# Performance work log

Measured on AMD Instinct MI355X. Metric: run time of the kernel, lower is better.

## Reference

```python
import jax, jax.numpy as jnp
import numpy as np

B, S, D, H, C = 64, 512, 768, 768, 5


def setup_inputs() -> dict:
    key = jax.random.key(0)
    ks = jax.random.split(key, 7)
    return {
        "hidden_states": jax.random.normal(ks[0], (B, S, D), jnp.float32),
        "mask": jnp.ones((B, S), dtype=bool),
        # Dense(hidden_size, relu)
        "W1": jax.random.normal(ks[1], (D, H), jnp.float32) * 0.02,
        "b1": jnp.zeros((H,), jnp.float32),
        # CRF inner dense -> potentials over num_classes
        "W2": jax.random.normal(ks[2], (H, C), jnp.float32) * 0.02,
        "b2": jnp.zeros((C,), jnp.float32),
        # CRF transition matrix and boundary energies (tfa use_boundary=True)
        "chain_kernel": jax.random.normal(ks[3], (C, C), jnp.float32) * 0.1,
        "left_boundary": jax.random.normal(ks[4], (C,), jnp.float32) * 0.1,
        "right_boundary": jax.random.normal(ks[5], (C,), jnp.float32) * 0.1,
    }


def viterbi_decode(potentials, trans):
    """potentials: [B,S,C], trans: [C,C] -> decoded tags [B,S] int32."""
    pot_t = jnp.swapaxes(potentials, 0, 1)  # [S,B,C]

    def fwd_step(alpha, pot):
        scores = alpha[:, :, None] + trans[None]      # [B,C_prev,C_cur]
        bp = jnp.argmax(scores, axis=1)               # [B,C]
        alpha = jnp.max(scores, axis=1) + pot         # [B,C]
        return alpha, bp

    alpha, bps = jax.lax.scan(fwd_step, pot_t[0], pot_t[1:])  # bps: [S-1,B,C]
    last = jnp.argmax(alpha, axis=-1).astype(jnp.int32)       # [B]

    def back_step(tag, bp):
        prev = jnp.take_along_axis(bp, tag[:, None], axis=1)[:, 0].astype(jnp.int32)
        return prev, prev

    _, tags = jax.lax.scan(back_step, last, bps, reverse=True)  # [S-1,B]
    decoded = jnp.concatenate([jnp.swapaxes(tags, 0, 1), last[:, None]], axis=1)
    return decoded


def reference(hidden_states, mask, W1, b1, W2, b2, chain_kernel,
              left_boundary, right_boundary):
    # Dense + ReLU (dropout is identity at inference / training=False)
    h = jax.nn.relu(jnp.einsum('bsd,dh->bsh', hidden_states, W1) + b1)
    # CRF inner dense -> unary potentials
    pot = jnp.einsum('bsh,hc->bsc', h, W2) + b2
    # boundary energies at first / last timestep (mask is full-length here)
    pot = pot.at[:, 0].add(left_boundary).at[:, -1].add(right_boundary)
    seq_length = jnp.sum(mask.astype(jnp.int32), axis=1)
    decoded = viterbi_decode(pot, chain_kernel)
    return decoded, pot, seq_length, chain_kernel
```

## Files before the change

### kernel.cpp

```cpp
#include <hip/hip_runtime.h>

#define B_  64
#define S_  512
#define D_  768
#define H_  768
#define C_  5
#define M_  (B_ * S_)

typedef float f32x4 __attribute__((ext_vector_type(4)));
typedef short short8 __attribute__((ext_vector_type(8)));

#define W1T_ELEMS (D_ * H_)
#define XBF_ELEMS (M_ * D_)

#define PX_BLOCKS   (XBF_ELEMS / (256 * 8))
#define PW_BLOCKS   ((D_ / 32) * (H_ / 32))
#define PI_BLOCKS   ((M_ * C_ + 255) / 256)

__device__ __forceinline__ unsigned short f2bf(float f) {
    unsigned int u = __float_as_uint(f);
    u += 0x7FFFu + ((u >> 16) & 1u);
    return (unsigned short)(u >> 16);
}

__global__ __launch_bounds__(256) void prep_all_kernel(
    const float* __restrict__ X, const float* __restrict__ W1,
    const float* __restrict__ b2, const float* __restrict__ lb,
    const float* __restrict__ rb,
    unsigned short* __restrict__ xbf, unsigned short* __restrict__ w1t,
    float* __restrict__ pot)
{
    __shared__ float t[32][33];
    const int bid = blockIdx.x;
    const int tid = threadIdx.x;

    if (bid < PX_BLOCKS) {
        const size_t i0 = ((size_t)bid * 256 + tid) * 8;
        const float4 a = *(const float4*)(X + i0);
        const float4 b = *(const float4*)(X + i0 + 4);
        union { unsigned short u[8]; uint4 v; } o;
        o.u[0] = f2bf(a.x); o.u[1] = f2bf(a.y); o.u[2] = f2bf(a.z); o.u[3] = f2bf(a.w);
        o.u[4] = f2bf(b.x); o.u[5] = f2bf(b.y); o.u[6] = f2bf(b.z); o.u[7] = f2bf(b.w);
        *(uint4*)(xbf + i0) = o.v;
    } else if (bid < PX_BLOCKS + PW_BLOCKS) {
        const int b2i = bid - PX_BLOCKS;
        const int bx = b2i % (H_ / 32);
        const int by = b2i / (H_ / 32);
        const int lx = tid & 31, ly = tid >> 5;
        #pragma unroll
        for (int j = 0; j < 4; ++j)
            t[ly + 8 * j][lx] = W1[(by * 32 + ly + 8 * j) * H_ + bx * 32 + lx];
        __syncthreads();
        #pragma unroll
        for (int j = 0; j < 4; ++j)
            w1t[(size_t)(bx * 32 + ly + 8 * j) * D_ + by * 32 + lx] = f2bf(t[lx][ly + 8 * j]);
    } else {
        const int idx = (bid - PX_BLOCKS - PW_BLOCKS) * 256 + tid;
        if (idx < M_ * C_) {
            const int c = idx % C_;
            const int tt = (idx / C_) & (S_ - 1);
            float v = b2[c];
            if (tt == 0)      v += lb[c];
            if (tt == S_ - 1) v += rb[c];
            pot[idx] = v;
        }
    }
}

__global__ __launch_bounds__(256) void prep_w1_kernel(
    const float* __restrict__ W1, unsigned short* __restrict__ w1t)
{
    __shared__ float t[32][33];
    const int bx = blockIdx.x, by = blockIdx.y;
    const int lx = threadIdx.x & 31, ly = threadIdx.x >> 5;
    #pragma unroll
    for (int j = 0; j < 4; ++j)
        t[ly + 8 * j][lx] = W1[(by * 32 + ly + 8 * j) * H_ + bx * 32 + lx];
    __syncthreads();
    #pragma unroll
    for (int j = 0; j < 4; ++j)
        w1t[(size_t)(bx * 32 + ly + 8 * j) * D_ + by * 32 + lx] = f2bf(t[lx][ly + 8 * j]);
}

__global__ __launch_bounds__(256) void init_pot_kernel(
    const float* __restrict__ b2, const float* __restrict__ lb,
    const float* __restrict__ rb, float* __restrict__ pot)
{
    const int idx = blockIdx.x * 256 + threadIdx.x;
    if (idx < M_ * C_) {
        const int c = idx % C_;
        const int t = (idx / C_) & (S_ - 1);
        float v = b2[c];
        if (t == 0)      v += lb[c];
        if (t == S_ - 1) v += rb[c];
        pot[idx] = v;
    }
}

__device__ __forceinline__ void gload16(const void* g, void* l) {
    __builtin_amdgcn_global_load_lds(
        (const __attribute__((address_space(1))) unsigned int*)g,
        (__attribute__((address_space(3))) unsigned int*)l, 16, 0, 0);
}

__global__ __launch_bounds__(256, 4) void gemm_sb_kernel(
    const unsigned short* __restrict__ xbf,
    const unsigned short* __restrict__ w1t,
    const float* __restrict__ b1,
    const float* __restrict__ W2,
    float* __restrict__ pot)
{
    __shared__ __align__(16) unsigned short Asm[8192];
    __shared__ __align__(16) unsigned short Bsm[8192];

    const int tid  = threadIdx.x;
    const int lane = tid & 63, w = tid >> 6;
    const int wm   = w >> 1, wn = w & 1;
    const int i15  = lane & 15, quad = lane >> 4;

    const int bid = blockIdx.x;
    const int r8 = bid & 7, q8 = bid >> 3;
    const int nb = q8 % 6, mhi = q8 / 6;
    const int m0 = (mhi * 8 + r8) * 128;
    const int n0 = nb * 128;

    const unsigned short* gA[2];
    const unsigned short* gB[2];
    int lofs[2];
    #pragma unroll
    for (int i = 0; i < 2; ++i) {
        const int g = 2 * w + i;
        gA[i] = xbf + (size_t)(m0 + g * 16 + i15) * D_ + quad * 8;
        gB[i] = w1t + (size_t)(n0 + g * 16 + i15) * D_ + quad * 8;
        lofs[i] = g * 512;
    }

    f32x4 acc[4][4];
    #pragma unroll
    for (int mi = 0; mi < 4; ++mi)
        #pragma unroll
        for (int ni = 0; ni < 4; ++ni)
            acc[mi][ni] = (f32x4){0.f, 0.f, 0.f, 0.f};

    #define KITERS (D_ / 64)
    for (int kt = 0; kt < KITERS; ++kt) {
        __syncthreads();
        #pragma unroll
        for (int i = 0; i < 2; ++i) {
            gload16(gA[i],      &Asm[lofs[i]]);
            gload16(gA[i] + 32, &Asm[4096 + lofs[i]]);
            gload16(gB[i],      &Bsm[lofs[i]]);
            gload16(gB[i] + 32, &Bsm[4096 + lofs[i]]);
            gA[i] += 64; gB[i] += 64;
        }
        __syncthreads();

        #pragma unroll
        for (int c = 0; c < 2; ++c) {
            const int cb = c * 4096;
            short8 af[4], bfr[4];
            #pragma unroll
            for (int mi = 0; mi < 4; ++mi)
                af[mi] = *(const short8*)&Asm[cb + (wm * 4 + mi) * 512 + quad * 128 + i15 * 8];
            #pragma unroll
            for (int ni = 0; ni < 4; ++ni)
                bfr[ni] = *(const short8*)&Bsm[cb + (wn * 4 + ni) * 512 + quad * 128 + i15 * 8];
            #pragma unroll
            for (int ni = 0; ni < 4; ++ni)
                #pragma unroll
                for (int mi = 0; mi < 4; ++mi)
                    acc[mi][ni] = __builtin_amdgcn_mfma_f32_16x16x32_bf16(
                        af[mi], bfr[ni], acc[mi][ni], 0, 0, 0);
        }
    }
    __syncthreads();

    float* pp = (float*)&Asm[0];

    float b1v[4], w2v[4][C_];
    #pragma unroll
    for (int ni = 0; ni < 4; ++ni) {
        const int col = n0 + wn * 64 + ni * 16 + i15;
        b1v[ni] = b1[col];
        #pragma unroll
        for (int cc = 0; cc < C_; ++cc) w2v[ni][cc] = W2[col * C_ + cc];
    }

    #pragma unroll
    for (int mi = 0; mi < 4; ++mi) {
        float ps[4][C_];
        #pragma unroll
        for (int r = 0; r < 4; ++r)
            #pragma unroll
            for (int cc = 0; cc < C_; ++cc) ps[r][cc] = 0.f;

        #pragma unroll
        for (int ni = 0; ni < 4; ++ni)
            #pragma unroll
            for (int r = 0; r < 4; ++r) {
                float h = acc[mi][ni][r] + b1v[ni];
                h = h > 0.f ? h : 0.f;
                #pragma unroll
                for (int cc = 0; cc < C_; ++cc)
                    ps[r][cc] = fmaf(h, w2v[ni][cc], ps[r][cc]);
            }

        #pragma unroll
        for (int off = 1; off < 16; off <<= 1)
            #pragma unroll
            for (int r = 0; r < 4; ++r)
                #pragma unroll
                for (int cc = 0; cc < C_; ++cc)
                    ps[r][cc] += __shfl_xor(ps[r][cc], off, 64);

        if (i15 == 0) {
            #pragma unroll
            for (int r = 0; r < 4; ++r) {
                const int row = wm * 64 + mi * 16 + quad * 4 + r;
                #pragma unroll
                for (int cc = 0; cc < C_; ++cc)
                    pp[(wn * 128 + row) * C_ + cc] = ps[r][cc];
            }
        }
    }
    __syncthreads();

    for (int idx = tid; idx < 128 * C_; idx += 256) {
        const int row = idx / C_, cc = idx % C_;
        atomicAdd(&pot[(size_t)(m0 + row) * C_ + cc],
                  pp[row * C_ + cc] + pp[(128 + row) * C_ + cc]);
    }
}

__global__ __launch_bounds__(256) void gemm_bf16_kernel(
    const float* __restrict__ X,
    const unsigned short* __restrict__ w1t,
    const float* __restrict__ b1,
    const float* __restrict__ W2,
    float* __restrict__ pot)
{
    __shared__ __align__(16) float          Asm[128 * 32];
    __shared__ __align__(16) unsigned short Bsm[128 * 32];
    __shared__ float pp[2][128][C_];

    const int tid  = threadIdx.x;
    const int lane = tid & 63, w = tid >> 6;
    const int wm   = w >> 1, wn = w & 1;
    const int i15  = lane & 15, quad = lane >> 4;

    const int bid = blockIdx.x;
    const int r8 = bid & 7, q8 = bid >> 3;
    const int nb = q8 % 6, mhi = q8 / 6;
    const int m0 = (mhi * 8 + r8) * 128;
    const int n0 = nb * 128;

    const float* gA[4];
    float* lA[4];
    const unsigned short* gB[2];
    unsigned short* lB[2];
    #pragma unroll
    for (int i = 0; i < 4; ++i) {
        const int a = 4 * w + i, g = a >> 1, h = a & 1;
        gA[i] = X + (size_t)(m0 + g * 16 + i15) * D_ + (4 * h + quad) * 4;
        lA[i] = &Asm[g * 512 + h * 256];
    }
    #pragma unroll
    for (int i = 0; i < 2; ++i) {
        const int b = 2 * w + i;
        gB[i] = w1t + (size_t)(n0 + b * 16 + i15) * D_ + quad * 8;
        lB[i] = &Bsm[b * 512];
    }

    f32x4 acc[4][4];
    #pragma unroll
    for (int mi = 0; mi < 4; ++mi)
        #pragma unroll
        for (int ni = 0; ni < 4; ++ni)
            acc[mi][ni] = (f32x4){0.f, 0.f, 0.f, 0.f};

    for (int kt = 0; kt < D_ / 32; ++kt) {
        __syncthreads();
        #pragma unroll
        for (int i = 0; i < 4; ++i) { gload16(gA[i], lA[i]); gA[i] += 32; }
        #pragma unroll
        for (int i = 0; i < 2; ++i) { gload16(gB[i], lB[i]); gB[i] += 32; }
        __syncthreads();

        short8 af[4];
        #pragma unroll
        for (int mi = 0; mi < 4; ++mi) {
            const int row = wm * 64 + mi * 16 + i15;
            const int base = (row >> 4) * 512 + (row & 15) * 4 + quad * 128;
            const f32x4 lo = *(const f32x4*)&Asm[base];
            const f32x4 hi = *(const f32x4*)&Asm[base + 64];
            float f[8];
            *(f32x4*)&f[0] = lo; *(f32x4*)&f[4] = hi;
            union { short8 s; unsigned short u[8]; } cv;
            #pragma unroll
            for (int j = 0; j < 8; ++j) cv.u[j] = f2bf(f[j]);
            af[mi] = cv.s;
        }
        short8 bfr[4];
        #pragma unroll
        for (int ni = 0; ni < 4; ++ni) {
            const int row = wn * 64 + ni * 16 + i15;
            bfr[ni] = *(const short8*)&Bsm[(row >> 4) * 512 + quad * 128 + (row & 15) * 8];
        }
        #pragma unroll
        for (int ni = 0; ni < 4; ++ni)
            #pragma unroll
            for (int mi = 0; mi < 4; ++mi)
                acc[mi][ni] = __builtin_amdgcn_mfma_f32_16x16x32_bf16(
                    af[mi], bfr[ni], acc[mi][ni], 0, 0, 0);
    }

    float b1v[4], w2v[4][C_];
    #pragma unroll
    for (int ni = 0; ni < 4; ++ni) {
        const int col = n0 + wn * 64 + ni * 16 + i15;
        b1v[ni] = b1[col];
        #pragma unroll
        for (int cc = 0; cc < C_; ++cc) w2v[ni][cc] = W2[col * C_ + cc];
    }

    #pragma unroll
    for (int mi = 0; mi < 4; ++mi) {
        float ps[4][C_];
        #pragma unroll
        for (int r = 0; r < 4; ++r)
            #pragma unroll
            for (int cc = 0; cc < C_; ++cc) ps[r][cc] = 0.f;

        #pragma unroll
        for (int ni = 0; ni < 4; ++ni)
            #pragma unroll
            for (int r = 0; r < 4; ++r) {
                float h = acc[mi][ni][r] + b1v[ni];
                h = h > 0.f ? h : 0.f;
                #pragma unroll
                for (int cc = 0; cc < C_; ++cc)
                    ps[r][cc] = fmaf(h, w2v[ni][cc], ps[r][cc]);
            }

        #pragma unroll
        for (int off = 1; off < 16; off <<= 1)
            #pragma unroll
            for (int r = 0; r < 4; ++r)
                #pragma unroll
                for (int cc = 0; cc < C_; ++cc)
                    ps[r][cc] += __shfl_xor(ps[r][cc], off, 64);

        if (i15 == 0) {
            #pragma unroll
            for (int r = 0; r < 4; ++r) {
                const int row = wm * 64 + mi * 16 + quad * 4 + r;
                #pragma unroll
                for (int cc = 0; cc < C_; ++cc)
                    pp[wn][row][cc] = ps[r][cc];
            }
        }
    }
    __syncthreads();

    for (int idx = tid; idx < 128 * C_; idx += 256) {
        const int row = idx / C_, cc = idx % C_;
        atomicAdd(&pot[(size_t)(m0 + row) * C_ + cc],
                  pp[0][row][cc] + pp[1][row][cc]);
    }
}

#define FBK 8
#define FLDS 132
__global__ __launch_bounds__(256) void gemm_relu_pot_kernel(
    const float* __restrict__ X, const float* __restrict__ W1,
    const float* __restrict__ b1, const float* __restrict__ W2,
    float* __restrict__ pot)
{
    __shared__ float As[FBK * FLDS];
    __shared__ float Bs[FBK * FLDS];
    __shared__ float w2s[128][C_];

    const int tid = threadIdx.x;
    const int tx = tid & 15, ty = tid >> 4;
    const int m0 = blockIdx.y * 128, n0 = blockIdx.x * 128;

    for (int idx = tid; idx < 128 * C_; idx += 256)
        w2s[idx / C_][idx % C_] = W2[(n0 + idx / C_) * C_ + idx % C_];

    float acc[2][2][4][4];
    #pragma unroll
    for (int a = 0; a < 2; ++a)
        #pragma unroll
        for (int b = 0; b < 2; ++b)
            #pragma unroll
            for (int i = 0; i < 4; ++i)
                #pragma unroll
                for (int j = 0; j < 4; ++j) acc[a][b][i][j] = 0.f;

    const int arow = tid >> 1, aq = tid & 1;
    const int brow = tid >> 5, bq = tid & 31;
    const float* Aptr = X + (m0 + arow) * D_ + aq * 4;
    const float* Bptr = W1 + brow * H_ + n0 + bq * 4;

    for (int kt = 0; kt < D_; kt += FBK) {
        const float4 avv = *(const float4*)Aptr;
        const float4 bvv = *(const float4*)Bptr;
        __syncthreads();
        As[(aq * 4 + 0) * FLDS + arow] = avv.x;
        As[(aq * 4 + 1) * FLDS + arow] = avv.y;
        As[(aq * 4 + 2) * FLDS + arow] = avv.z;
        As[(aq * 4 + 3) * FLDS + arow] = avv.w;
        *(float4*)&Bs[brow * FLDS + bq * 4] = bvv;
        __syncthreads();
        #pragma unroll
        for (int k = 0; k < FBK; ++k) {
            const float4 a0 = *(const float4*)&As[k * FLDS + (ty << 2)];
            const float4 a1 = *(const float4*)&As[k * FLDS + 64 + (ty << 2)];
            const float4 b0 = *(const float4*)&Bs[k * FLDS + (tx << 2)];
            const float4 b1r = *(const float4*)&Bs[k * FLDS + 64 + (tx << 2)];
            const float ar[2][4] = {{a0.x,a0.y,a0.z,a0.w},{a1.x,a1.y,a1.z,a1.w}};
            const float br[2][4] = {{b0.x,b0.y,b0.z,b0.w},{b1r.x,b1r.y,b1r.z,b1r.w}};
            #pragma unroll
            for (int ri = 0; ri < 2; ++ri)
                #pragma unroll
                for (int i = 0; i < 4; ++i)
                    #pragma unroll
                    for (int rj = 0; rj < 2; ++rj)
                        #pragma unroll
                        for (int j = 0; j < 4; ++j)
                            acc[ri][rj][i][j] = fmaf(ar[ri][i], br[rj][j], acc[ri][rj][i][j]);
        }
        Aptr += FBK;
        Bptr += FBK * H_;
    }

    float ps[2][4][C_];
    #pragma unroll
    for (int ri = 0; ri < 2; ++ri)
        #pragma unroll
        for (int i = 0; i < 4; ++i)
            #pragma unroll
            for (int cc = 0; cc < C_; ++cc) ps[ri][i][cc] = 0.f;

    #pragma unroll
    for (int rj = 0; rj < 2; ++rj)
        #pragma unroll
        for (int j = 0; j < 4; ++j) {
            const int nl = rj * 64 + (tx << 2) + j;
            const float bj = b1[n0 + nl];
            float w2c[C_];
            #pragma unroll
            for (int cc = 0; cc < C_; ++cc) w2c[cc] = w2s[nl][cc];
            #pragma unroll
            for (int ri = 0; ri < 2; ++ri)
                #pragma unroll
                for (int i = 0; i < 4; ++i) {
                    float h = acc[ri][rj][i][j] + bj;
                    h = h > 0.f ? h : 0.f;
                    #pragma unroll
                    for (int cc = 0; cc < C_; ++cc)
                        ps[ri][i][cc] = fmaf(h, w2c[cc], ps[ri][i][cc]);
                }
        }

    #pragma unroll
    for (int off = 1; off < 16; off <<= 1)
        #pragma unroll
        for (int ri = 0; ri < 2; ++ri)
            #pragma unroll
            for (int i = 0; i < 4; ++i)
                #pragma unroll
                for (int cc = 0; cc < C_; ++cc)
                    ps[ri][i][cc] += __shfl_xor(ps[ri][i][cc], off, 64);

    if (tx == 0)
        #pragma unroll
        for (int ri = 0; ri < 2; ++ri)
            #pragma unroll
            for (int i = 0; i < 4; ++i) {
                const int m = m0 + ri * 64 + (ty << 2) + i;
                #pragma unroll
                for (int cc = 0; cc < C_; ++cc)
                    atomicAdd(&pot[m * C_ + cc], ps[ri][i][cc]);
            }
}

__global__ __launch_bounds__(64) void viterbi_kernel(
    const float* __restrict__ pot, const float* __restrict__ trans,
    const int* __restrict__ mask, float* __restrict__ decoded,
    float* __restrict__ seqlen, float* __restrict__ chain_out)
{
    const int b = blockIdx.x;
    const int lane = threadIdx.x;

    __shared__ float pl[S_ * C_];
    __shared__ unsigned int bpk[S_];
    __shared__ unsigned int gseg[64];
    __shared__ int bt[64];
    __shared__ int dec_s[S_];
    __shared__ int s_last;

    const float* pb = pot + b * (S_ * C_);
    for (int i = lane; i < S_ * C_; i += 64) pl[i] = pb[i];

    int mcnt = 0;
    const int* mb = mask + b * S_;
    for (int i = lane; i < S_; i += 64) mcnt += (mb[i] != 0) ? 1 : 0;
    #pragma unroll
    for (int off = 32; off >= 1; off >>= 1) mcnt += __shfl_xor(mcnt, off, 64);

    if (b == 0 && lane < C_ * C_) chain_out[lane] = trans[lane];

    float tr[C_][C_];
    #pragma unroll
    for (int p = 0; p < C_; ++p)
        #pragma unroll
        for (int c = 0; c < C_; ++c) tr[p][c] = trans[p * C_ + c];

    __syncthreads();

    const float NEG = -1.0e30f;

    float G[C_][C_];
    #pragma unroll
    for (int c = 0; c < C_; ++c)
        #pragma unroll
        for (int p = 0; p < C_; ++p) G[c][p] = (c == p) ? 0.f : NEG;

    for (int j = 1; j <= 8; ++j) {
        const int t = 8 * lane + j;
        if (t < S_) {
            float ng[C_][C_];
            #pragma unroll
            for (int c = 0; c < C_; ++c) {
                const float pc = pl[t * C_ + c];
                #pragma unroll
                for (int p = 0; p < C_; ++p) {
                    float m = tr[0][c] + G[0][p];
                    #pragma unroll
                    for (int q = 1; q < C_; ++q)
                        m = fmaxf(m, tr[q][c] + G[q][p]);
                    ng[c][p] = m + pc;
                }
            }
            #pragma unroll
            for (int c = 0; c < C_; ++c)
                #pragma unroll
                for (int p = 0; p < C_; ++p) G[c][p] = ng[c][p];
        }
    }

    #pragma unroll
    for (int d = 1; d < 64; d <<= 1) {
        float Q[C_][C_];
        #pragma unroll
        for (int q = 0; q < C_; ++q)
            #pragma unroll
            for (int p = 0; p < C_; ++p) Q[q][p] = __shfl_up(G[q][p], d, 64);
        if (lane >= d) {
            float ng[C_][C_];
            #pragma unroll
            for (int c = 0; c < C_; ++c)
                #pragma unroll
                for (int p = 0; p < C_; ++p) {
                    float m = G[c][0] + Q[0][p];
                    #pragma unroll
                    for (int q = 1; q < C_; ++q)
                        m = fmaxf(m, G[c][q] + Q[q][p]);
                    ng[c][p] = m;
                }
            #pragma unroll
            for (int c = 0; c < C_; ++c)
                #pragma unroll
                for (int p = 0; p < C_; ++p) G[c][p] = ng[c][p];
        }
    }

    float a[C_];
    {
        float E[C_][C_];
        #pragma unroll
        for (int c = 0; c < C_; ++c)
            #pragma unroll
            for (int p = 0; p < C_; ++p) E[c][p] = __shfl_up(G[c][p], 1, 64);
        float a0[C_];
        #pragma unroll
        for (int c = 0; c < C_; ++c) a0[c] = pl[c];
        if (lane == 0) {
            #pragma unroll
            for (int c = 0; c < C_; ++c) a[c] = a0[c];
        } else {
            #pragma unroll
            for (int c = 0; c < C_; ++c) {
                float m = E[c][0] + a0[0];
                #pragma unroll
                for (int q = 1; q < C_; ++q) m = fmaxf(m, E[c][q] + a0[q]);
                a[c] = m;
            }
        }
    }

    for (int j = 1; j <= 8; ++j) {
        const int t = 8 * lane + j;
        if (t < S_) {
            unsigned int mpack = 0;
            float na[C_];
            #pragma unroll
            for (int c = 0; c < C_; ++c) {
                float best = a[0] + tr[0][c];
                int arg = 0;
                #pragma unroll
                for (int p = 1; p < C_; ++p) {
                    const float s = a[p] + tr[p][c];
                    if (s > best) { best = s; arg = p; }
                }
                mpack |= (unsigned int)arg << (3 * c);
                na[c] = best + pl[t * C_ + c];
            }
            bpk[t] = mpack;
            #pragma unroll
            for (int c = 0; c < C_; ++c) a[c] = na[c];
        }
    }

    if (lane == 63) {
        float best = a[0];
        int arg = 0;
        #pragma unroll
        for (int p = 1; p < C_; ++p)
            if (a[p] > best) { best = a[p]; arg = p; }
        s_last = arg;
    }
    if (lane == 0) bpk[0] = 0;
    __syncthreads();

    const int last = s_last;

    unsigned int g = 0u | (1u << 3) | (2u << 6) | (3u << 9) | (4u << 12);
    #pragma unroll
    for (int j = 7; j >= 0; --j) {
        const int t = 8 * lane + j;
        if (t >= 1) {
            const unsigned int m = bpk[t];
            unsigned int ng = 0;
            #pragma unroll
            for (int x = 0; x < C_; ++x) {
                const unsigned int gx = (g >> (3 * x)) & 7u;
                ng |= ((m >> (3 * gx)) & 7u) << (3 * x);
            }
            g = ng;
        }
    }
    gseg[lane] = g;
    __syncthreads();

    if (lane == 0) {
        int cur = last;
        for (int l = 63; l >= 0; --l) {
            bt[l] = cur;
            cur = (int)((gseg[l] >> (3 * cur)) & 7u);
        }
        seqlen[b] = (float)mcnt;
    }
    __syncthreads();

    {
        int tag = bt[lane];
        const int t0 = 8 * lane;
        dec_s[t0 + 7] = tag;
        #pragma unroll
        for (int t = t0 + 7; t >= t0 + 1; --t) {
            tag = (int)((bpk[t] >> (3 * tag)) & 7u);
            dec_s[t - 1] = tag;
        }
    }
    __syncthreads();

    float* db = decoded + b * S_;
    for (int i = lane; i < S_; i += 64) db[i] = (float)dec_s[i];
}

extern "C" void kernel_launch(void* const* d_in, const int* in_sizes, int n_in,
                              void* d_out, int out_size, void* d_ws, size_t ws_size,
                              hipStream_t stream) {
    const float* hs    = (const float*)d_in[0];
    const int*   mask  = (const int*)  d_in[1];
    const float* W1    = (const float*)d_in[2];
    const float* b1    = (const float*)d_in[3];
    const float* W2    = (const float*)d_in[4];
    const float* b2    = (const float*)d_in[5];
    const float* chain = (const float*)d_in[6];
    const float* lb    = (const float*)d_in[7];
    const float* rb    = (const float*)d_in[8];

    float* out      = (float*)d_out;
    float* decoded  = out;
    float* pot      = out + M_;
    float* seq      = out + M_ + M_ * C_;
    float* chainout = seq + B_;

    const size_t need_w1 = (size_t)W1T_ELEMS * sizeof(unsigned short);
    const size_t need_all = need_w1 + (size_t)XBF_ELEMS * sizeof(unsigned short);

    if (ws_size >= need_all) {
        unsigned short* w1t = (unsigned short*)d_ws;
        unsigned short* xbf = w1t + W1T_ELEMS;
        prep_all_kernel<<<PX_BLOCKS + PW_BLOCKS + PI_BLOCKS, 256, 0, stream>>>(
            hs, W1, b2, lb, rb, xbf, w1t, pot);
        gemm_sb_kernel<<<1536, 256, 0, stream>>>(xbf, w1t, b1, W2, pot);
    } else if (ws_size >= need_w1) {
        unsigned short* w1t = (unsigned short*)d_ws;
        init_pot_kernel<<<PI_BLOCKS, 256, 0, stream>>>(b2, lb, rb, pot);
        dim3 pgrid(H_ / 32, D_ / 32);
        prep_w1_kernel<<<pgrid, 256, 0, stream>>>(W1, w1t);
        gemm_bf16_kernel<<<1536, 256, 0, stream>>>(hs, w1t, b1, W2, pot);
    } else {
        init_pot_kernel<<<PI_BLOCKS, 256, 0, stream>>>(b2, lb, rb, pot);
        dim3 grid(H_ / 128, M_ / 128);
        gemm_relu_pot_kernel<<<grid, 256, 0, stream>>>(hs, W1, b1, W2, pot);
    }

    viterbi_kernel<<<B_, 64, 0, stream>>>(pot, chain, mask, decoded, seq, chainout);
}
```

Measured before the change: 277.1 us.

## Fuse X bf16 conversion into full-N GEMM tile and drop atomics

Replaces the separate X-to-bf16 prep pass and the 128x128 tiled GEMM with one kernel. Each 512-thread block owns 64 rows across the whole hidden dimension (768 columns), converts X to bf16 on the fly while staging it into LDS, and writes pot directly with b2 and the boundary terms folded in, so no atomics and no init pass are needed. This removes the round trip of writing and re-reading a bf16 copy of X. In exchange each block holds a large B tile in LDS (about 96KB), which may limit occupancy, and the single-buffered staging leaves little overlap of loads with MFMA work.

```diff
diff --git a/kernel.cpp b/kernel.cpp
--- a/kernel.cpp
+++ b/kernel.cpp
@@ -11,11 +11,6 @@
 typedef short short8 __attribute__((ext_vector_type(8)));
 
 #define W1T_ELEMS (D_ * H_)
-#define XBF_ELEMS (M_ * D_)
-
-#define PX_BLOCKS   (XBF_ELEMS / (256 * 8))
-#define PW_BLOCKS   ((D_ / 32) * (H_ / 32))
-#define PI_BLOCKS   ((M_ * C_ + 255) / 256)
 
 __device__ __forceinline__ unsigned short f2bf(float f) {
     unsigned int u = __float_as_uint(f);
@@ -23,48 +18,10 @@
     return (unsigned short)(u >> 16);
 }
 
-__global__ __launch_bounds__(256) void prep_all_kernel(
-    const float* __restrict__ X, const float* __restrict__ W1,
-    const float* __restrict__ b2, const float* __restrict__ lb,
-    const float* __restrict__ rb,
-    unsigned short* __restrict__ xbf, unsigned short* __restrict__ w1t,
-    float* __restrict__ pot)
-{
-    __shared__ float t[32][33];
-    const int bid = blockIdx.x;
-    const int tid = threadIdx.x;
-
-    if (bid < PX_BLOCKS) {
-        const size_t i0 = ((size_t)bid * 256 + tid) * 8;
-        const float4 a = *(const float4*)(X + i0);
-        const float4 b = *(const float4*)(X + i0 + 4);
-        union { unsigned short u[8]; uint4 v; } o;
-        o.u[0] = f2bf(a.x); o.u[1] = f2bf(a.y); o.u[2] = f2bf(a.z); o.u[3] = f2bf(a.w);
-        o.u[4] = f2bf(b.x); o.u[5] = f2bf(b.y); o.u[6] = f2bf(b.z); o.u[7] = f2bf(b.w);
-        *(uint4*)(xbf + i0) = o.v;
-    } else if (bid < PX_BLOCKS + PW_BLOCKS) {
-        const int b2i = bid - PX_BLOCKS;
-        const int bx = b2i % (H_ / 32);
-        const int by = b2i / (H_ / 32);
-        const int lx = tid & 31, ly = tid >> 5;
-        #pragma unroll
-        for (int j = 0; j < 4; ++j)
-            t[ly + 8 * j][lx] = W1[(by * 32 + ly + 8 * j) * H_ + bx * 32 + lx];
-        __syncthreads();
-        #pragma unroll
-        for (int j = 0; j < 4; ++j)
-            w1t[(size_t)(bx * 32 + ly + 8 * j) * D_ + by * 32 + lx] = f2bf(t[lx][ly + 8 * j]);
-    } else {
-        const int idx = (bid - PX_BLOCKS - PW_BLOCKS) * 256 + tid;
-        if (idx < M_ * C_) {
-            const int c = idx % C_;
-            const int tt = (idx / C_) & (S_ - 1);
-            float v = b2[c];
-            if (tt == 0)      v += lb[c];
-            if (tt == S_ - 1) v += rb[c];
-            pot[idx] = v;
-        }
-    }
+__device__ __forceinline__ void gload16(const void* g, void* l) {
+    __builtin_amdgcn_global_load_lds(
+        (const __attribute__((address_space(1))) unsigned int*)g,
+        (__attribute__((address_space(3))) unsigned int*)l, 16, 0, 0);
 }
 
 __global__ __launch_bounds__(256) void prep_w1_kernel(
@@ -97,227 +54,93 @@
     }
 }
 
-__device__ __forceinline__ void gload16(const void* g, void* l) {
-    __builtin_amdgcn_global_load_lds(
-        (const __attribute__((address_space(1))) unsigned int*)g,
-        (__attribute__((address_space(3))) unsigned int*)l, 16, 0, 0);
-}
-
-__global__ __launch_bounds__(256, 4) void gemm_sb_kernel(
-    const unsigned short* __restrict__ xbf,
-    const unsigned short* __restrict__ w1t,
-    const float* __restrict__ b1,
-    const float* __restrict__ W2,
-    float* __restrict__ pot)
-{
-    __shared__ __align__(16) unsigned short Asm[8192];
-    __shared__ __align__(16) unsigned short Bsm[8192];
-
-    const int tid  = threadIdx.x;
-    const int lane = tid & 63, w = tid >> 6;
-    const int wm   = w >> 1, wn = w & 1;
-    const int i15  = lane & 15, quad = lane >> 4;
-
-    const int bid = blockIdx.x;
-    const int r8 = bid & 7, q8 = bid >> 3;
-    const int nb = q8 % 6, mhi = q8 / 6;
-    const int m0 = (mhi * 8 + r8) * 128;
-    const int n0 = nb * 128;
-
-    const unsigned short* gA[2];
-    const unsigned short* gB[2];
-    int lofs[2];
-    #pragma unroll
-    for (int i = 0; i < 2; ++i) {
-        const int g = 2 * w + i;
-        gA[i] = xbf + (size_t)(m0 + g * 16 + i15) * D_ + quad * 8;
-        gB[i] = w1t + (size_t)(n0 + g * 16 + i15) * D_ + quad * 8;
-        lofs[i] = g * 512;
-    }
-
-    f32x4 acc[4][4];
-    #pragma unroll
-    for (int mi = 0; mi < 4; ++mi)
-        #pragma unroll
-        for (int ni = 0; ni < 4; ++ni)
-            acc[mi][ni] = (f32x4){0.f, 0.f, 0.f, 0.f};
-
-    #define KITERS (D_ / 64)
-    for (int kt = 0; kt < KITERS; ++kt) {
-        __syncthreads();
-        #pragma unroll
-        for (int i = 0; i < 2; ++i) {
-            gload16(gA[i],      &Asm[lofs[i]]);
-            gload16(gA[i] + 32, &Asm[4096 + lofs[i]]);
-            gload16(gB[i],      &Bsm[lofs[i]]);
-            gload16(gB[i] + 32, &Bsm[4096 + lofs[i]]);
-            gA[i] += 64; gB[i] += 64;
-        }
-        __syncthreads();
-
-        #pragma unroll
-        for (int c = 0; c < 2; ++c) {
-            const int cb = c * 4096;
-            short8 af[4], bfr[4];
-            #pragma unroll
-            for (int mi = 0; mi < 4; ++mi)
-                af[mi] = *(const short8*)&Asm[cb + (wm * 4 + mi) * 512 + quad * 128 + i15 * 8];
-            #pragma unroll
-            for (int ni = 0; ni < 4; ++ni)
-                bfr[ni] = *(const short8*)&Bsm[cb + (wn * 4 + ni) * 512 + quad * 128 + i15 * 8];
-            #pragma unroll
-            for (int ni = 0; ni < 4; ++ni)
-                #pragma unroll
-                for (int mi = 0; mi < 4; ++mi)
-                    acc[mi][ni] = __builtin_amdgcn_mfma_f32_16x16x32_bf16(
-                        af[mi], bfr[ni], acc[mi][ni], 0, 0, 0);
-        }
-    }
-    __syncthreads();
-
-    float* pp = (float*)&Asm[0];
-
-    float b1v[4], w2v[4][C_];
-    #pragma unroll
-    for (int ni = 0; ni < 4; ++ni) {
-        const int col = n0 + wn * 64 + ni * 16 + i15;
-        b1v[ni] = b1[col];
-        #pragma unroll
-        for (int cc = 0; cc < C_; ++cc) w2v[ni][cc] = W2[col * C_ + cc];
-    }
-
-    #pragma unroll
-    for (int mi = 0; mi < 4; ++mi) {
-        float ps[4][C_];
-        #pragma unroll
-        for (int r = 0; r < 4; ++r)
-            #pragma unroll
-            for (int cc = 0; cc < C_; ++cc) ps[r][cc] = 0.f;
-
-        #pragma unroll
-        for (int ni = 0; ni < 4; ++ni)
-            #pragma unroll
-            for (int r = 0; r < 4; ++r) {
-                float h = acc[mi][ni][r] + b1v[ni];
-                h = h > 0.f ? h : 0.f;
-                #pragma unroll
-                for (int cc = 0; cc < C_; ++cc)
-                    ps[r][cc] = fmaf(h, w2v[ni][cc], ps[r][cc]);
-            }
-
-        #pragma unroll
-        for (int off = 1; off < 16; off <<= 1)
-            #pragma unroll
-            for (int r = 0; r < 4; ++r)
-                #pragma unroll
-                for (int cc = 0; cc < C_; ++cc)
-                    ps[r][cc] += __shfl_xor(ps[r][cc], off, 64);
-
-        if (i15 == 0) {
-            #pragma unroll
-            for (int r = 0; r < 4; ++r) {
-                const int row = wm * 64 + mi * 16 + quad * 4 + r;
-                #pragma unroll
-                for (int cc = 0; cc < C_; ++cc)
-                    pp[(wn * 128 + row) * C_ + cc] = ps[r][cc];
-            }
-        }
-    }
-    __syncthreads();
-
-    for (int idx = tid; idx < 128 * C_; idx += 256) {
-        const int row = idx / C_, cc = idx % C_;
-        atomicAdd(&pot[(size_t)(m0 + row) * C_ + cc],
-                  pp[row * C_ + cc] + pp[(128 + row) * C_ + cc]);
-    }
-}
-
-__global__ __launch_bounds__(256) void gemm_bf16_kernel(
+__global__ __launch_bounds__(512, 2) void gemm_fulln_kernel(
     const float* __restrict__ X,
     const unsigned short* __restrict__ w1t,
     const float* __restrict__ b1,
     const float* __restrict__ W2,
+    const float* __restrict__ b2,
+    const float* __restrict__ lb,
+    const float* __restrict__ rb,
     float* __restrict__ pot)
 {
-    __shared__ __align__(16) float          Asm[128 * 32];
-    __shared__ __align__(16) unsigned short Bsm[128 * 32];
-    __shared__ float pp[2][128][C_];
+    __shared__ __align__(16) unsigned short Alds[4 * 2 * 512];
+    __shared__ __align__(16) unsigned short Blds[48 * 2 * 512];
 
     const int tid  = threadIdx.x;
     const int lane = tid & 63, w = tid >> 6;
-    const int wm   = w >> 1, wn = w & 1;
     const int i15  = lane & 15, quad = lane >> 4;
-
-    const int bid = blockIdx.x;
-    const int r8 = bid & 7, q8 = bid >> 3;
-    const int nb = q8 % 6, mhi = q8 / 6;
-    const int m0 = (mhi * 8 + r8) * 128;
-    const int n0 = nb * 128;
-
-    const float* gA[4];
-    float* lA[4];
-    const unsigned short* gB[2];
-    unsigned short* lB[2];
-    #pragma unroll
-    for (int i = 0; i < 4; ++i) {
-        const int a = 4 * w + i, g = a >> 1, h = a & 1;
-        gA[i] = X + (size_t)(m0 + g * 16 + i15) * D_ + (4 * h + quad) * 4;
-        lA[i] = &Asm[g * 512 + h * 256];
-    }
-    #pragma unroll
-    for (int i = 0; i < 2; ++i) {
-        const int b = 2 * w + i;
-        gB[i] = w1t + (size_t)(n0 + b * 16 + i15) * D_ + quad * 8;
-        lB[i] = &Bsm[b * 512];
-    }
-
-    f32x4 acc[4][4];
+    const int m0   = blockIdx.x * 64;
+
+    const int arow = tid >> 3;
+    const int ak0  = (tid & 7) * 8;
+    const float* aSrc = X + (size_t)(m0 + arow) * D_ + ak0;
+    unsigned short* aDst = &Alds[((arow >> 4) * 2 + (ak0 >> 5)) * 512
+                                 + ((ak0 >> 3) & 3) * 128 + (arow & 15) * 8];
+
+    const unsigned short* bSrc = w1t + (size_t)(6 * w * 16 + i15) * D_ + quad * 8;
+
+    f32x4 acc[4][6];
     #pragma unroll
     for (int mi = 0; mi < 4; ++mi)
         #pragma unroll
-        for (int ni = 0; ni < 4; ++ni)
+        for (int ni = 0; ni < 6; ++ni)
             acc[mi][ni] = (f32x4){0.f, 0.f, 0.f, 0.f};
 
-    for (int kt = 0; kt < D_ / 32; ++kt) {
+    #define STAGE(KB) do {                                                   \
+        _Pragma("unroll")                                                    \
+        for (int gi = 0; gi < 6; ++gi) {                                     \
+            const unsigned short* s = bSrc + (size_t)gi * 16 * D_ + (KB);    \
+            gload16(s,      &Blds[((6 * w + gi) * 2 + 0) * 512]);            \
+            gload16(s + 32, &Blds[((6 * w + gi) * 2 + 1) * 512]);            \
+        }                                                                    \
+        {                                                                    \
+            const float4 x0 = *(const float4*)(aSrc + (KB));                 \
+            const float4 x1 = *(const float4*)(aSrc + (KB) + 4);             \
+            union { unsigned short u[8]; uint4 v; } o;                       \
+            o.u[0] = f2bf(x0.x); o.u[1] = f2bf(x0.y);                        \
+            o.u[2] = f2bf(x0.z); o.u[3] = f2bf(x0.w);                        \
+            o.u[4] = f2bf(x1.x); o.u[5] = f2bf(x1.y);                        \
+            o.u[6] = f2bf(x1.z); o.u[7] = f2bf(x1.w);                        \
+            *(uint4*)aDst = o.v;                                             \
+        }                                                                    \
+    } while (0)
+
+    STAGE(0);
+    #define KSTEPS (D_ / 64)
+    for (int kt = 0; kt < KSTEPS; ++kt) {
         __syncthreads();
-        #pragma unroll
-        for (int i = 0; i < 4; ++i) { gload16(gA[i], lA[i]); gA[i] += 32; }
-        #pragma unroll
-        for (int i = 0; i < 2; ++i) { gload16(gB[i], lB[i]); gB[i] += 32; }
-        __syncthreads();
-
-        short8 af[4];
-        #pragma unroll
-        for (int mi = 0; mi < 4; ++mi) {
-            const int row = wm * 64 + mi * 16 + i15;
-            const int base = (row >> 4) * 512 + (row & 15) * 4 + quad * 128;
-            const f32x4 lo = *(const f32x4*)&Asm[base];
-            const f32x4 hi = *(const f32x4*)&Asm[base + 64];
-            float f[8];
-            *(f32x4*)&f[0] = lo; *(f32x4*)&f[4] = hi;
-            union { short8 s; unsigned short u[8]; } cv;
-            #pragma unroll
-            for (int j = 0; j < 8; ++j) cv.u[j] = f2bf(f[j]);
-            af[mi] = cv.s;
-        }
-        short8 bfr[4];
-        #pragma unroll
-        for (int ni = 0; ni < 4; ++ni) {
-            const int row = wn * 64 + ni * 16 + i15;
-            bfr[ni] = *(const short8*)&Bsm[(row >> 4) * 512 + quad * 128 + (row & 15) * 8];
-        }
-        #pragma unroll
-        for (int ni = 0; ni < 4; ++ni)
+
+        #pragma unroll
+        for (int kh = 0; kh < 2; ++kh) {
+            short8 af[4], bfr[6];
             #pragma unroll
             for (int mi = 0; mi < 4; ++mi)
-                acc[mi][ni] = __builtin_amdgcn_mfma_f32_16x16x32_bf16(
-                    af[mi], bfr[ni], acc[mi][ni], 0, 0, 0);
-    }
-
-    float b1v[4], w2v[4][C_];
-    #pragma unroll
-    for (int ni = 0; ni < 4; ++ni) {
-        const int col = n0 + wn * 64 + ni * 16 + i15;
+                af[mi] = *(const short8*)&Alds[(mi * 2 + kh) * 512 + lane * 8];
+            #pragma unroll
+            for (int ni = 0; ni < 6; ++ni)
+                bfr[ni] = *(const short8*)&Blds[((w * 6 + ni) * 2 + kh) * 512 + lane * 8];
+            #pragma unroll
+            for (int ni = 0; ni < 6; ++ni)
+                #pragma unroll
+                for (int mi = 0; mi < 4; ++mi)
+                    acc[mi][ni] = __builtin_amdgcn_mfma_f32_16x16x32_bf16(
+                        af[mi], bfr[ni], acc[mi][ni], 0, 0, 0);
+        }
+
+        if (kt + 1 < KSTEPS) {
+            __syncthreads();
+            STAGE((kt + 1) * 64);
+        }
+    }
+    __syncthreads();
+
+    float* pp = (float*)&Blds[0];
+
+    float b1v[6], w2v[6][C_];
+    #pragma unroll
+    for (int ni = 0; ni < 6; ++ni) {
+        const int col = w * 96 + ni * 16 + i15;
         b1v[ni] = b1[col];
         #pragma unroll
         for (int cc = 0; cc < C_; ++cc) w2v[ni][cc] = W2[col * C_ + cc];
@@ -332,7 +155,7 @@
             for (int cc = 0; cc < C_; ++cc) ps[r][cc] = 0.f;
 
         #pragma unroll
-        for (int ni = 0; ni < 4; ++ni)
+        for (int ni = 0; ni < 6; ++ni)
             #pragma unroll
             for (int r = 0; r < 4; ++r) {
                 float h = acc[mi][ni][r] + b1v[ni];
@@ -353,19 +176,26 @@
         if (i15 == 0) {
             #pragma unroll
             for (int r = 0; r < 4; ++r) {
-                const int row = wm * 64 + mi * 16 + quad * 4 + r;
+                const int row = mi * 16 + quad * 4 + r;
                 #pragma unroll
                 for (int cc = 0; cc < C_; ++cc)
-                    pp[wn][row][cc] = ps[r][cc];
-            }
-        }
-    }
-    __syncthreads();
-
-    for (int idx = tid; idx < 128 * C_; idx += 256) {
+                    pp[(w * 64 + row) * C_ + cc] = ps[r][cc];
+            }
+        }
+    }
+    __syncthreads();
+
+    for (int idx = tid; idx < 64 * C_; idx += 512) {
         const int row = idx / C_, cc = idx % C_;
-        atomicAdd(&pot[(size_t)(m0 + row) * C_ + cc],
-                  pp[0][row][cc] + pp[1][row][cc]);
+        float s = b2[cc];
+        #pragma unroll
+        for (int wv = 0; wv < 8; ++wv)
+            s += pp[(wv * 64 + row) * C_ + cc];
+        const int gm = m0 + row;
+        const int tt = gm & (S_ - 1);
+        if (tt == 0)      s += lb[cc];
+        if (tt == S_ - 1) s += rb[cc];
+        pot[(size_t)gm * C_ + cc] = s;
     }
 }
 
@@ -700,21 +530,15 @@
     float* chainout = seq + B_;
 
     const size_t need_w1 = (size_t)W1T_ELEMS * sizeof(unsigned short);
-    const size_t need_all = need_w1 + (size_t)XBF_ELEMS * sizeof(unsigned short);
-
-    if (ws_size >= need_all) {
+
+    if (ws_size >= need_w1) {
         unsigned short* w1t = (unsigned short*)d_ws;
-        unsigned short* xbf = w1t + W1T_ELEMS;
-        prep_all_kernel<<<PX_BLOCKS + PW_BLOCKS + PI_BLOCKS, 256, 0, stream>>>(
-            hs, W1, b2, lb, rb, xbf, w1t, pot);
-        gemm_sb_kernel<<<1536, 256, 0, stream>>>(xbf, w1t, b1, W2, pot);
-    } else if (ws_size >= need_w1) {
-        unsigned short* w1t = (unsigned short*)d_ws;
-        init_pot_kernel<<<PI_BLOCKS, 256, 0, stream>>>(b2, lb, rb, pot);
         dim3 pgrid(H_ / 32, D_ / 32);
         prep_w1_kernel<<<pgrid, 256, 0, stream>>>(W1, w1t);
-        gemm_bf16_kernel<<<1536, 256, 0, stream>>>(hs, w1t, b1, W2, pot);
+        gemm_fulln_kernel<<<M_ / 64, 512, 0, stream>>>(
+            hs, w1t, b1, W2, b2, lb, rb, pot);
     } else {
+        const int PI_BLOCKS = (M_ * C_ + 255) / 256;
         init_pot_kernel<<<PI_BLOCKS, 256, 0, stream>>>(b2, lb, rb, pot);
         dim3 grid(H_ / 128, M_ / 128);
         gemm_relu_pot_kernel<<<grid, 256, 0, stream>>>(hs, W1, b1, W2, pot);
```

Result: faster. 271.4 us (-2.0%).
